# Optimization experiments

Hardware: AMD Instinct MI355X
Metric: run time of the kernel (lower is better)

## Reference

```python
import jax, jax.numpy as jnp
import numpy as np

LABEL_NUM = 32      # distinct identities in the batch
K = 16              # samples per class per modality
MODALITIES = 3      # feats is chunked into label_num*3 groups
M = LABEL_NUM * K * MODALITIES   # 1536 total samples
N = LABEL_NUM * MODALITIES       # 96 centers (one per chunk)
STRIPES = 8         # local horizontal stripes
D_LOCAL = 1024      # per-stripe local feature dim
FEAT_DIM = STRIPES * D_LOCAL     # 8192 global feature dim
MARGIN = 0.3


def setup_inputs() -> dict:
    key = jax.random.key(0)
    k1, k2 = jax.random.split(key)
    feats = jax.random.normal(k1, (M, FEAT_DIM), dtype=jnp.float32)
    # chunk-structured labels: each contiguous block of K samples shares a label,
    # pattern repeated for each of the 3 modality streams
    labels = jnp.tile(jnp.repeat(jnp.arange(LABEL_NUM, dtype=jnp.int32), K), MODALITIES)
    local_features = jax.random.normal(k2, (M, D_LOCAL, STRIPES), dtype=jnp.float32)
    return {"feats": feats, "labels": labels, "local_features": local_features}


def _pdist(a, b):
    # euclidean distance matrix [m, n] (matches pdist_torch incl. 1e-12 clamp)
    d2 = (jnp.sum(a * a, axis=1)[:, None]
          + jnp.sum(b * b, axis=1)[None, :]
          - 2.0 * (a @ b.T))
    return jnp.sqrt(jnp.clip(d2, 1e-12, None))


def _batch_euclidean_dist(x, y):
    # x: [B, m, d], y: [B, n, d] -> [B, m, n]
    d2 = (jnp.sum(x * x, axis=-1)[:, :, None]
          + jnp.sum(y * y, axis=-1)[:, None, :]
          - 2.0 * jnp.einsum('bmd,bnd->bmn', x, y))
    return jnp.sqrt(jnp.clip(d2, 1e-12, None))


def _shortest_dist(d):
    # d: [B, m, n]; AlignedReID shortest-path DP over the (m, n) grid -> [B]
    mm, nn = d.shape[1], d.shape[2]
    dp = [[None] * nn for _ in range(mm)]
    for i in range(mm):
        for j in range(nn):
            if i == 0 and j == 0:
                dp[i][j] = d[:, i, j]
            elif i == 0:
                dp[i][j] = dp[i][j - 1] + d[:, i, j]
            elif j == 0:
                dp[i][j] = dp[i - 1][j] + d[:, i, j]
            else:
                dp[i][j] = jnp.minimum(dp[i - 1][j], dp[i][j - 1]) + d[:, i, j]
    return dp[-1][-1]


def _batch_local_dist(x, y):
    d = _batch_euclidean_dist(x, y)
    d = (jnp.exp(d) - 1.0) / (jnp.exp(d) + 1.0)  # normalize to (0, 1)
    return _shortest_dist(d)


def reference(feats, labels, local_features):
    m = feats.shape[0]          # 1536
    n = N                       # 96 chunks/centers
    k = m // n                  # 16 samples per chunk
    # per-chunk centers (mean over each contiguous chunk of feats)
    centers = feats.reshape(n, k, -1).mean(axis=1)          # [N, D]
    dist = _pdist(centers, feats)                           # [N, M]
    anchor_labels = labels[::k]                             # label of each chunk, [N]
    is_pos = anchor_labels[:, None] == labels[None, :]      # [N, M]
    masked_pos = jnp.where(is_pos, dist, -jnp.inf)
    p_inds = jnp.argmax(masked_pos, axis=1)                 # hardest positive per center
    masked_neg = jnp.where(is_pos, jnp.inf, dist)
    n_inds = jnp.argmin(masked_neg, axis=1)                 # hardest negative per center
    lf = jnp.transpose(local_features, (0, 2, 1))           # [M, stripes, d_local]
    p_local = lf[p_inds]                                    # [N, stripes, d_local]
    n_local = lf[n_inds]
    inputs1 = centers.reshape(n, STRIPES, -1)               # [N, stripes, d_local]
    local_dist_ap = _batch_local_dist(inputs1, p_local)     # [N]
    local_dist_an = _batch_local_dist(inputs1, n_local)     # [N]
    # MarginRankingLoss(x1=an, x2=ap, y=1): mean(relu(ap - an + margin))
    loss = jnp.mean(jax.nn.relu(local_dist_ap - local_dist_an + MARGIN))
    return loss
```

## Files before the change

kernel.cpp:

```cpp
#include <hip/hip_runtime.h>
#include <math.h>

#define M_ROWS 1536
#define NC 96
#define KG 16
#define FD 8192
#define NS 8
#define MARGIN 0.3f

#define KSPLIT 32
#define KCH 256
#define BKS 32
#define NST (KCH / BKS)
#define BN 64

typedef short v8s __attribute__((ext_vector_type(8)));
typedef float v4f __attribute__((ext_vector_type(4)));

__device__ __forceinline__ void split4t(float4 v, ushort4* h, ushort4* l) {
    const unsigned int ux = __float_as_uint(v.x), uy = __float_as_uint(v.y);
    const unsigned int uz = __float_as_uint(v.z), uw = __float_as_uint(v.w);
    *h = make_ushort4((unsigned short)(ux >> 16), (unsigned short)(uy >> 16),
                      (unsigned short)(uz >> 16), (unsigned short)(uw >> 16));
    const float rx = v.x - __uint_as_float(ux & 0xffff0000u);
    const float ry = v.y - __uint_as_float(uy & 0xffff0000u);
    const float rz = v.z - __uint_as_float(uz & 0xffff0000u);
    const float rw = v.w - __uint_as_float(uw & 0xffff0000u);
    *l = make_ushort4((unsigned short)(__float_as_uint(rx) >> 16),
                      (unsigned short)(__float_as_uint(ry) >> 16),
                      (unsigned short)(__float_as_uint(rz) >> 16),
                      (unsigned short)(__float_as_uint(rw) >> 16));
}

__global__ void centers_kernel(const float* __restrict__ feats,
                               float* __restrict__ centers,
                               float* __restrict__ fnp,
                               float* __restrict__ cnp) {
    const int c = blockIdx.x;
    const int bd = blockIdx.y;
    const int tid = threadIdx.x;

    float sq[KG];
#pragma unroll
    for (int k = 0; k < KG; ++k) sq[k] = 0.f;
    float cp = 0.f;

#pragma unroll
    for (int it = 0; it < 2; ++it) {
        const int base = bd * 2048 + it * 1024 + tid * 4;
        float4 acc = make_float4(0.f, 0.f, 0.f, 0.f);
#pragma unroll
        for (int k = 0; k < KG; ++k) {
            const float4 v = *(const float4*)&feats[(size_t)(c * KG + k) * FD + base];
            acc.x += v.x; acc.y += v.y; acc.z += v.z; acc.w += v.w;
            sq[k] += v.x * v.x + v.y * v.y + v.z * v.z + v.w * v.w;
        }
        float4 cv = make_float4(acc.x * 0.0625f, acc.y * 0.0625f,
                                acc.z * 0.0625f, acc.w * 0.0625f);
        *(float4*)&centers[(size_t)c * FD + base] = cv;
        cp += cv.x * cv.x + cv.y * cv.y + cv.z * cv.z + cv.w * cv.w;
    }

    const int lane = tid & 63;
    const int w = tid >> 6;
    __shared__ float wred[4][17];
#pragma unroll
    for (int k = 0; k < KG; ++k) {
        float v = sq[k];
#pragma unroll
        for (int off = 32; off > 0; off >>= 1) v += __shfl_down(v, off, 64);
        if (lane == 0) wred[w][k] = v;
    }
    {
        float v = cp;
#pragma unroll
        for (int off = 32; off > 0; off >>= 1) v += __shfl_down(v, off, 64);
        if (lane == 0) wred[w][16] = v;
    }
    __syncthreads();
    if (tid < 17) {
        const float t = wred[0][tid] + wred[1][tid] + wred[2][tid] + wred[3][tid];
        if (tid < 16) fnp[bd * M_ROWS + c * KG + tid] = t;
        else          cnp[bd * NC + c] = t;
    }
}

__global__ __launch_bounds__(256) void gemm11_kernel(const float* __restrict__ centers,
                                                     const float* __restrict__ feats,
                                                     float* __restrict__ part) {
    const int bid = blockIdx.x;
    const int ks = bid & 31;
    const int nb = bid >> 5;
    const int tid = threadIdx.x;
    const int j0 = nb * BN;
    const int k0b = ks * KCH;

    __shared__ unsigned short AH[2][6 * 512], AL[2][6 * 512];
    __shared__ unsigned short BH[2][4 * 512], BL[2][4 * 512];

    int aoff[3], aidx[3];
#pragma unroll
    for (int i = 0; i < 3; ++i) {
        const int q = tid + i * 256;
        const int m = q >> 3, kk = (q & 7) * 4;
        aoff[i] = m * FD + kk;
        aidx[i] = (m >> 4) * 512 + ((m & 15) | ((kk >> 3) << 4)) * 8 + (kk & 7);
    }
    int boff[2], bidx[2];
#pragma unroll
    for (int i = 0; i < 2; ++i) {
        const int q = tid + i * 256;
        const int n = q >> 3, kk = (q & 7) * 4;
        boff[i] = (j0 + n) * FD + kk;
        bidx[i] = (n >> 4) * 512 + ((n & 15) | ((kk >> 3) << 4)) * 8 + (kk & 7);
    }

    float4 pa[3], pb[2];
#pragma unroll
    for (int i = 0; i < 3; ++i) pa[i] = *(const float4*)&centers[aoff[i] + k0b];
#pragma unroll
    for (int i = 0; i < 2; ++i) pb[i] = *(const float4*)&feats[boff[i] + k0b];
#pragma unroll
    for (int i = 0; i < 3; ++i) {
        ushort4 h, l; split4t(pa[i], &h, &l);
        *(ushort4*)&AH[0][aidx[i]] = h; *(ushort4*)&AL[0][aidx[i]] = l;
    }
#pragma unroll
    for (int i = 0; i < 2; ++i) {
        ushort4 h, l; split4t(pb[i], &h, &l);
        *(ushort4*)&BH[0][bidx[i]] = h; *(ushort4*)&BL[0][bidx[i]] = l;
    }
    __syncthreads();

    v4f acc[3][2];
#pragma unroll
    for (int a = 0; a < 3; ++a)
#pragma unroll
        for (int b = 0; b < 2; ++b) {
            acc[a][b][0] = 0.f; acc[a][b][1] = 0.f;
            acc[a][b][2] = 0.f; acc[a][b][3] = 0.f;
        }

    const int w = tid >> 6, lane = tid & 63;
    const int wm = w >> 1, wn = w & 1;
    const int fo = lane * 8;

    int cur = 0;
    for (int st = 0; st < NST; ++st) {
        if (st < NST - 1) {
            const int k0 = k0b + (st + 1) * BKS;
#pragma unroll
            for (int i = 0; i < 3; ++i) pa[i] = *(const float4*)&centers[aoff[i] + k0];
#pragma unroll
            for (int i = 0; i < 2; ++i) pb[i] = *(const float4*)&feats[boff[i] + k0];
        }

        v8s Bhf[2], Blf[2];
#pragma unroll
        for (int nt = 0; nt < 2; ++nt) {
            Bhf[nt] = *(const v8s*)&BH[cur][(wn * 2 + nt) * 512 + fo];
            Blf[nt] = *(const v8s*)&BL[cur][(wn * 2 + nt) * 512 + fo];
        }
#pragma unroll
        for (int mt = 0; mt < 3; ++mt) {
            const v8s Ahf = *(const v8s*)&AH[cur][(wm * 3 + mt) * 512 + fo];
            const v8s Alf = *(const v8s*)&AL[cur][(wm * 3 + mt) * 512 + fo];
#pragma unroll
            for (int nt = 0; nt < 2; ++nt) {
                acc[mt][nt] = __builtin_amdgcn_mfma_f32_16x16x32_bf16(Ahf, Bhf[nt], acc[mt][nt], 0, 0, 0);
                acc[mt][nt] = __builtin_amdgcn_mfma_f32_16x16x32_bf16(Ahf, Blf[nt], acc[mt][nt], 0, 0, 0);
                acc[mt][nt] = __builtin_amdgcn_mfma_f32_16x16x32_bf16(Alf, Bhf[nt], acc[mt][nt], 0, 0, 0);
            }
        }

        if (st < NST - 1) {
            const int d = cur ^ 1;
#pragma unroll
            for (int i = 0; i < 3; ++i) {
                ushort4 h, l; split4t(pa[i], &h, &l);
                *(ushort4*)&AH[d][aidx[i]] = h; *(ushort4*)&AL[d][aidx[i]] = l;
            }
#pragma unroll
            for (int i = 0; i < 2; ++i) {
                ushort4 h, l; split4t(pb[i], &h, &l);
                *(ushort4*)&BH[d][bidx[i]] = h; *(ushort4*)&BL[d][bidx[i]] = l;
            }
        }
        __syncthreads();
        cur ^= 1;
    }

    const int col = lane & 15, r0 = (lane >> 4) * 4;
#pragma unroll
    for (int mt = 0; mt < 3; ++mt) {
#pragma unroll
        for (int nt = 0; nt < 2; ++nt) {
            const int n = j0 + (wn * 2 + nt) * 16 + col;
#pragma unroll
            for (int j = 0; j < 4; ++j) {
                const int m = (wm * 3 + mt) * 16 + r0 + j;
                part[((size_t)m * KSPLIT + ks) * M_ROWS + n] = acc[mt][nt][j];
            }
        }
    }
}

__global__ __launch_bounds__(512) void select_kernel(const float* __restrict__ part,
                                                     const float* __restrict__ fnp,
                                                     const float* __restrict__ cnp,
                                                     const int* __restrict__ labels,
                                                     int* __restrict__ pinds,
                                                     int* __restrict__ ninds) {
    const int c = blockIdx.x;
    const int tid = threadIdx.x;
    const int anchor = labels[c * KG];

    float cn = 0.f;
#pragma unroll
    for (int b = 0; b < 4; ++b) cn += cnp[b * NC + c];

    float bestp = -INFINITY; int bpi = 1 << 30;
    float bestn =  INFINITY; int bni = 1 << 30;

    const float* pc = part + (size_t)c * KSPLIT * M_ROWS;
    for (int j = tid; j < M_ROWS; j += 512) {
        float dot = 0.f;
#pragma unroll
        for (int p = 0; p < KSPLIT; ++p)
            dot += pc[(size_t)p * M_ROWS + j];
        float fn = 0.f;
#pragma unroll
        for (int b = 0; b < 4; ++b) fn += fnp[b * M_ROWS + j];
        const float d2 = cn + fn - 2.f * dot;
        const bool pos = (labels[j] == anchor);
        if (pos) {
            if (d2 > bestp || (d2 == bestp && j < bpi)) { bestp = d2; bpi = j; }
        } else {
            if (d2 < bestn || (d2 == bestn && j < bni)) { bestn = d2; bni = j; }
        }
    }

    __shared__ float sv[512];
    __shared__ int   si[512];
    sv[tid] = bestp; si[tid] = bpi; __syncthreads();
    for (int s = 256; s > 0; s >>= 1) {
        if (tid < s) {
            if (sv[tid + s] > sv[tid] ||
                (sv[tid + s] == sv[tid] && si[tid + s] < si[tid])) {
                sv[tid] = sv[tid + s]; si[tid] = si[tid + s];
            }
        }
        __syncthreads();
    }
    if (tid == 0) pinds[c] = si[0];
    __syncthreads();
    sv[tid] = bestn; si[tid] = bni; __syncthreads();
    for (int s = 256; s > 0; s >>= 1) {
        if (tid < s) {
            if (sv[tid + s] < sv[tid] ||
                (sv[tid + s] == sv[tid] && si[tid + s] < si[tid])) {
                sv[tid] = sv[tid + s]; si[tid] = si[tid + s];
            }
        }
        __syncthreads();
    }
    if (tid == 0) ninds[c] = si[0];
}

__global__ void local_kernel(const float* __restrict__ centers,
                             const float* __restrict__ localf,
                             const int* __restrict__ pinds,
                             const int* __restrict__ ninds,
                             float* __restrict__ res) {
    const int c = blockIdx.x;
    const int which = blockIdx.y;
    const int tid = threadIdx.x;
    const int idx = (which == 0) ? pinds[c] : ninds[c];

    __shared__ float xl[NS * 1028];
    __shared__ float yl[NS * 1032];
    __shared__ float sred[256];
    __shared__ float dmat[64];
    __shared__ float xx[8], yy[8], xyv[64];

#pragma unroll
    for (int it = 0; it < 8; ++it) {
        const int q = tid + it * 256;
        const float4 v = *(const float4*)&centers[(size_t)c * FD + q * 4];
        const int i = q >> 8;
        const int d = (q * 4) & 1023;
        *(float4*)&xl[i * 1028 + d] = v;

        const float4 w = *(const float4*)&localf[(size_t)idx * FD + q * 4];
        const int jb = (q * 4) & 7;
        const int dd = q >> 1;
        yl[(jb + 0) * 1032 + dd] = w.x;
        yl[(jb + 1) * 1032 + dd] = w.y;
        yl[(jb + 2) * 1032 + dd] = w.z;
        yl[(jb + 3) * 1032 + dd] = w.w;
    }
    __syncthreads();

    const int p = tid >> 2, c4 = tid & 3;
    const int i = p >> 3, j = p & 7;
    float s = 0.f;
    for (int t = 0; t < 64; ++t) {
        const int d = c4 * 4 + t * 16;
        const float4 xv = *(const float4*)&xl[i * 1028 + d];
        const float4 yv = *(const float4*)&yl[j * 1032 + d];
        s += xv.x * yv.x + xv.y * yv.y + xv.z * yv.z + xv.w * yv.w;
    }
    sred[tid] = s;
    __syncthreads();
    if (tid < 64)
        xyv[tid] = sred[tid * 4] + sred[tid * 4 + 1] + sred[tid * 4 + 2] + sred[tid * 4 + 3];

    float s2 = 0.f;
    if (tid < 64) {
        const int r = tid >> 2;
        const float* base = (r < 8) ? &xl[r * 1028] : &yl[(r - 8) * 1032];
        for (int t = 0; t < 64; ++t) {
            const int d = c4 * 4 + t * 16;
            const float4 v = *(const float4*)&base[d];
            s2 += v.x * v.x + v.y * v.y + v.z * v.z + v.w * v.w;
        }
    }
    __syncthreads();
    sred[tid] = s2;
    __syncthreads();
    if (tid < 16) {
        const float v = sred[tid * 4] + sred[tid * 4 + 1] + sred[tid * 4 + 2] + sred[tid * 4 + 3];
        if (tid < 8) xx[tid] = v; else yy[tid - 8] = v;
    }
    __syncthreads();

    if (tid < 64) {
        const float d2 = xx[i] + yy[j] - 2.f * xyv[tid];
        const float d = sqrtf(fmaxf(d2, 1e-12f));
        dmat[tid] = tanhf(0.5f * d);
    }
    __syncthreads();

    if (tid == 0) {
        float prev[8], cur[8];
        cur[0] = dmat[0];
#pragma unroll
        for (int jj = 1; jj < 8; ++jj) cur[jj] = cur[jj - 1] + dmat[jj];
        for (int ii = 1; ii < 8; ++ii) {
#pragma unroll
            for (int jj = 0; jj < 8; ++jj) prev[jj] = cur[jj];
            cur[0] = prev[0] + dmat[ii * 8];
#pragma unroll
            for (int jj = 1; jj < 8; ++jj)
                cur[jj] = fminf(prev[jj], cur[jj - 1]) + dmat[ii * 8 + jj];
        }
        res[which * NC + c] = cur[7];
    }
}

__global__ void loss_kernel(const float* __restrict__ res, float* __restrict__ out) {
    const int tid = threadIdx.x;
    float v = 0.f;
    if (tid < NC) v = fmaxf(res[tid] - res[NC + tid] + MARGIN, 0.f);
#pragma unroll
    for (int off = 32; off > 0; off >>= 1) v += __shfl_down(v, off, 64);
    __shared__ float w2[2];
    const int lane = tid & 63, w = tid >> 6;
    if (lane == 0) w2[w] = v;
    __syncthreads();
    if (tid == 0) out[0] = (w2[0] + w2[1]) * (1.f / NC);
}

extern "C" void kernel_launch(void* const* d_in, const int* in_sizes, int n_in,
                              void* d_out, int out_size, void* d_ws, size_t ws_size,
                              hipStream_t stream) {
    const float* feats  = (const float*)d_in[0];
    const int*   labels = (const int*)d_in[1];
    const float* localf = (const float*)d_in[2];
    float* out = (float*)d_out;

    float* centers = (float*)d_ws;
    float* part    = centers + (size_t)NC * FD;
    float* fnp     = part + (size_t)NC * KSPLIT * M_ROWS;
    float* cnp     = fnp + 4 * M_ROWS;
    float* res     = cnp + 4 * NC;
    int*   pinds   = (int*)(res + 2 * NC);
    int*   ninds   = pinds + NC;

    hipLaunchKernelGGL(centers_kernel, dim3(NC, 4), dim3(256), 0, stream,
                       feats, centers, fnp, cnp);
    hipLaunchKernelGGL(gemm11_kernel, dim3(24 * KSPLIT), dim3(256), 0, stream,
                       centers, feats, part);
    hipLaunchKernelGGL(select_kernel, dim3(NC), dim3(512), 0, stream,
                       part, fnp, cnp, labels, pinds, ninds);
    hipLaunchKernelGGL(local_kernel, dim3(NC, 2), dim3(256), 0, stream,
                       centers, localf, pinds, ninds, res);
    hipLaunchKernelGGL(loss_kernel, dim3(1), dim3(128), 0, stream, res, out);
}
```

Baseline: 50.88 us.

## Pre-split centers into bf16 hi/lo fragment layout in centers kernel

The centers kernel now also writes the bf16 high and low parts of each center, stored directly in the per-lane MFMA fragment order. The GEMM kernel then loads its A operands straight from global memory into registers, with no LDS staging and no per-block split. This removes the A-side shared-memory traffic and the split work that each of the 24 N-blocks was repeating. In exchange there are extra global writes in the centers kernel and un-prefetched global loads of A inside the main loop.

```diff
diff --git a/kernel.cpp b/kernel.cpp
--- a/kernel.cpp
+++ b/kernel.cpp
@@ -34,6 +34,8 @@
 
 __global__ void centers_kernel(const float* __restrict__ feats,
                                float* __restrict__ centers,
+                               unsigned short* __restrict__ ch,
+                               unsigned short* __restrict__ cl,
                                float* __restrict__ fnp,
                                float* __restrict__ cnp) {
     const int c = blockIdx.x;
@@ -58,6 +60,14 @@
         float4 cv = make_float4(acc.x * 0.0625f, acc.y * 0.0625f,
                                 acc.z * 0.0625f, acc.w * 0.0625f);
         *(float4*)&centers[(size_t)c * FD + base] = cv;
+        {
+            ushort4 h, l; split4t(cv, &h, &l);
+            const int kb = base >> 5;
+            const int ln = (c & 15) | (((base >> 3) & 3) << 4);
+            const size_t off = ((size_t)(kb * 6 + (c >> 4)) * 64 + ln) * 8 + (base & 7);
+            *(ushort4*)&ch[off] = h;
+            *(ushort4*)&cl[off] = l;
+        }
         cp += cv.x * cv.x + cv.y * cv.y + cv.z * cv.z + cv.w * cv.w;
     }
 
@@ -85,7 +95,8 @@
     }
 }
 
-__global__ __launch_bounds__(256) void gemm11_kernel(const float* __restrict__ centers,
+__global__ __launch_bounds__(256) void gemm15_kernel(const unsigned short* __restrict__ ch,
+                                                     const unsigned short* __restrict__ cl,
                                                      const float* __restrict__ feats,
                                                      float* __restrict__ part) {
     const int bid = blockIdx.x;
@@ -95,17 +106,8 @@
     const int j0 = nb * BN;
     const int k0b = ks * KCH;
 
-    __shared__ unsigned short AH[2][6 * 512], AL[2][6 * 512];
     __shared__ unsigned short BH[2][4 * 512], BL[2][4 * 512];
 
-    int aoff[3], aidx[3];
-#pragma unroll
-    for (int i = 0; i < 3; ++i) {
-        const int q = tid + i * 256;
-        const int m = q >> 3, kk = (q & 7) * 4;
-        aoff[i] = m * FD + kk;
-        aidx[i] = (m >> 4) * 512 + ((m & 15) | ((kk >> 3) << 4)) * 8 + (kk & 7);
-    }
     int boff[2], bidx[2];
 #pragma unroll
     for (int i = 0; i < 2; ++i) {
@@ -115,16 +117,9 @@
         bidx[i] = (n >> 4) * 512 + ((n & 15) | ((kk >> 3) << 4)) * 8 + (kk & 7);
     }
 
-    float4 pa[3], pb[2];
-#pragma unroll
-    for (int i = 0; i < 3; ++i) pa[i] = *(const float4*)&centers[aoff[i] + k0b];
+    float4 pb[2];
 #pragma unroll
     for (int i = 0; i < 2; ++i) pb[i] = *(const float4*)&feats[boff[i] + k0b];
-#pragma unroll
-    for (int i = 0; i < 3; ++i) {
-        ushort4 h, l; split4t(pa[i], &h, &l);
-        *(ushort4*)&AH[0][aidx[i]] = h; *(ushort4*)&AL[0][aidx[i]] = l;
-    }
 #pragma unroll
     for (int i = 0; i < 2; ++i) {
         ushort4 h, l; split4t(pb[i], &h, &l);
@@ -144,13 +139,20 @@
     const int w = tid >> 6, lane = tid & 63;
     const int wm = w >> 1, wn = w & 1;
     const int fo = lane * 8;
+    const int kb0 = k0b >> 5;
 
     int cur = 0;
+#pragma unroll
     for (int st = 0; st < NST; ++st) {
+        v8s Ah[3], Al[3];
+#pragma unroll
+        for (int mt = 0; mt < 3; ++mt) {
+            const size_t o = (((size_t)(kb0 + st) * 6 + wm * 3 + mt) * 64 + lane) * 8;
+            Ah[mt] = *(const v8s*)&ch[o];
+            Al[mt] = *(const v8s*)&cl[o];
+        }
         if (st < NST - 1) {
             const int k0 = k0b + (st + 1) * BKS;
-#pragma unroll
-            for (int i = 0; i < 3; ++i) pa[i] = *(const float4*)&centers[aoff[i] + k0];
 #pragma unroll
             for (int i = 0; i < 2; ++i) pb[i] = *(const float4*)&feats[boff[i] + k0];
         }
@@ -163,23 +165,16 @@
         }
 #pragma unroll
         for (int mt = 0; mt < 3; ++mt) {
-            const v8s Ahf = *(const v8s*)&AH[cur][(wm * 3 + mt) * 512 + fo];
-            const v8s Alf = *(const v8s*)&AL[cur][(wm * 3 + mt) * 512 + fo];
 #pragma unroll
             for (int nt = 0; nt < 2; ++nt) {
-                acc[mt][nt] = __builtin_amdgcn_mfma_f32_16x16x32_bf16(Ahf, Bhf[nt], acc[mt][nt], 0, 0, 0);
-                acc[mt][nt] = __builtin_amdgcn_mfma_f32_16x16x32_bf16(Ahf, Blf[nt], acc[mt][nt], 0, 0, 0);
-                acc[mt][nt] = __builtin_amdgcn_mfma_f32_16x16x32_bf16(Alf, Bhf[nt], acc[mt][nt], 0, 0, 0);
+                acc[mt][nt] = __builtin_amdgcn_mfma_f32_16x16x32_bf16(Ah[mt], Bhf[nt], acc[mt][nt], 0, 0, 0);
+                acc[mt][nt] = __builtin_amdgcn_mfma_f32_16x16x32_bf16(Ah[mt], Blf[nt], acc[mt][nt], 0, 0, 0);
+                acc[mt][nt] = __builtin_amdgcn_mfma_f32_16x16x32_bf16(Al[mt], Bhf[nt], acc[mt][nt], 0, 0, 0);
             }
         }
 
         if (st < NST - 1) {
             const int d = cur ^ 1;
-#pragma unroll
-            for (int i = 0; i < 3; ++i) {
-                ushort4 h, l; split4t(pa[i], &h, &l);
-                *(ushort4*)&AH[d][aidx[i]] = h; *(ushort4*)&AL[d][aidx[i]] = l;
-            }
 #pragma unroll
             for (int i = 0; i < 2; ++i) {
                 ushort4 h, l; split4t(pb[i], &h, &l);
@@ -384,13 +379,15 @@
     float* fnp     = part + (size_t)NC * KSPLIT * M_ROWS;
     float* cnp     = fnp + 4 * M_ROWS;
     float* res     = cnp + 4 * NC;
-    int*   pinds   = (int*)(res + 2 * NC);
+    unsigned short* ch = (unsigned short*)(res + 2 * NC);
+    unsigned short* cl = ch + (size_t)NC * FD;
+    int*   pinds   = (int*)(cl + (size_t)NC * FD);
     int*   ninds   = pinds + NC;
 
     hipLaunchKernelGGL(centers_kernel, dim3(NC, 4), dim3(256), 0, stream,
-                       feats, centers, fnp, cnp);
-    hipLaunchKernelGGL(gemm11_kernel, dim3(24 * KSPLIT), dim3(256), 0, stream,
-                       centers, feats, part);
+                       feats, centers, ch, cl, fnp, cnp);
+    hipLaunchKernelGGL(gemm15_kernel, dim3(24 * KSPLIT), dim3(256), 0, stream,
+                       ch, cl, feats, part);
     hipLaunchKernelGGL(select_kernel, dim3(NC), dim3(512), 0, stream,
                        part, fnp, cnp, labels, pinds, ninds);
     hipLaunchKernelGGL(local_kernel, dim3(NC, 2), dim3(256), 0, stream,
```

Measured after the change: 53.58 us. +5.3%, slower.
